# Kernel optimization log

Measured on AMD Instinct MI355X. Metric: run time of the kernel, lower is better.

## Reference

```python
import jax, jax.numpy as jnp
import numpy as np

NUM_INPUTS = 100          # nodes 0..99 have no in-edges (consume x)
NUM_HIDDEN = 501          # nodes 100..600, each with fan-in 4
FAN_IN = 4


def _make_edges():
    # Deterministic DAG: hidden node i = 100+k draws 4 distinct predecessors from [0, i)
    rs = np.random.RandomState(42)
    rows = np.stack([rs.choice(NUM_INPUTS + k, size=FAN_IN, replace=False)
                     for k in range(NUM_HIDDEN)]).astype(np.int32)
    return jnp.asarray(rows)


def setup_inputs() -> dict:
    key = jax.random.key(0)
    k_x, k_wi, k_bi, k_wh, k_bh = jax.random.split(key, 5)
    s = 1.0 / np.sqrt(FAN_IN)
    return {
        "x": jax.random.normal(k_x, (NUM_INPUTS,), dtype=jnp.float32),
        "w_in": jax.random.uniform(k_wi, (NUM_INPUTS,), jnp.float32, -1.0, 1.0),
        "b_in": jax.random.uniform(k_bi, (NUM_INPUTS,), jnp.float32, -1.0, 1.0),
        "w_hid": jax.random.uniform(k_wh, (NUM_HIDDEN, FAN_IN), jnp.float32, -s, s),
        "b_hid": jax.random.uniform(k_bh, (NUM_HIDDEN,), jnp.float32, -s, s),
        "edge_idx": _make_edges(),  # [501, 4] int32, row k indexes nodes < 100+k
    }


def reference(x, w_in, b_in, w_hid, b_hid, edge_idx):
    n_in = x.shape[0]
    total = n_in + edge_idx.shape[0]  # 601 nodes
    # Input nodes: sigmoid(Linear(1,1)(x[a])) for each a, vectorized.
    vals_in = jax.nn.sigmoid(w_in * x + b_in)  # [100]
    values = jnp.zeros((total,), x.dtype).at[:n_in].set(vals_in)
    node_ids = jnp.arange(n_in, total)

    def step(values, inp):
        idx, w, b, i = inp
        # cat of predecessor outputs -> Linear(4,1) -> sigmoid
        v = jax.nn.sigmoid(jnp.dot(w, values[idx]) + b)
        return values.at[i].set(v), None

    values, _ = jax.lax.scan(step, values, (edge_idx, w_hid, b_hid, node_ids))
    return values[-1:]  # values[number_of_nodes], shape [1]
```

## Files before the change

kernel.cpp:

```cpp
#include <hip/hip_runtime.h>


#define NUM_IN  100
#define NUM_HID 501
#define TOTAL   601

__launch_bounds__(64, 1)
__global__ void dag_kernel(const float* __restrict__ x,
                           const float* __restrict__ w_in,
                           const float* __restrict__ b_in,
                           const float* __restrict__ w_hid,
                           const float* __restrict__ b_hid,
                           const int*   __restrict__ edge_idx,
                           float* __restrict__ out) {
    __shared__ float vals[TOTAL];
    const int lane = threadIdx.x;

#define LOADP(J)                                                              \
    int4   e##J = make_int4(0, 0, 0, 0);                                      \
    float4 w##J = make_float4(0.f, 0.f, 0.f, 0.f);                            \
    float  b##J = 0.f;                                                        \
    bool   d##J;                                                              \
    {                                                                         \
        int k = (J) * 64 + lane;                                              \
        d##J = (k >= NUM_HID);        \
        if (k < NUM_HID) {                                                    \
            e##J = ((const int4*)edge_idx)[k];                                \
            w##J = ((const float4*)w_hid)[k];                                 \
            b##J = b_hid[k];                                                  \
        }                                                                     \
    }

    LOADP(0) LOADP(1) LOADP(2) LOADP(3) LOADP(4) LOADP(5) LOADP(6) LOADP(7)

    {
        float s = fmaf(w_in[lane], x[lane], b_in[lane]);
        vals[lane] = __builtin_amdgcn_rcpf(1.0f + __expf(-s));
    }
    if (lane < NUM_IN - 64) {
        int i = 64 + lane;
        float s = fmaf(w_in[i], x[i], b_in[i]);
        vals[i] = __builtin_amdgcn_rcpf(1.0f + __expf(-s));
    }
    #pragma unroll
    for (int j = 0; j < 8; ++j) {
        int kk = j * 64 + lane;
        if (kk < NUM_HID) vals[NUM_IN + kk] = -1.0f;
    }
    __builtin_amdgcn_wave_barrier();

#define SLOT(J)                                                               \
    if (!__all((int)d##J)) {                                                  \
        if (!d##J) {                                                          \
            float v0 = vals[e##J.x];                                          \
            float v1 = vals[e##J.y];                                          \
            float v2 = vals[e##J.z];                                          \
            float v3 = vals[e##J.w];                                          \
            int ready = ~((__float_as_int(v0) | __float_as_int(v1) |          \
                           __float_as_int(v2) | __float_as_int(v3))) >> 31;   \
            if (ready & 1) {                                                  \
                float s = fmaf(w##J.x, v0,                                    \
                          fmaf(w##J.y, v1,                                    \
                          fmaf(w##J.z, v2,                                    \
                          fmaf(w##J.w, v3, b##J))));                          \
                vals[NUM_IN + (J) * 64 + lane] =                              \
                    __builtin_amdgcn_rcpf(1.0f + __expf(-s));                 \
                d##J = true;                                                  \
            }                                                                 \
        }                                                                     \
    }                                                                         \
    __builtin_amdgcn_wave_barrier();

    bool alldone = false;
    #pragma unroll 1
    for (int sw = 0; sw < 64 && !alldone; ++sw) {
        SLOT(0) SLOT(1) SLOT(2) SLOT(3) SLOT(4) SLOT(5) SLOT(6) SLOT(7)
        alldone = __all((int)(d0 & d1 & d2 & d3 & d4 & d5 & d6 & d7));
    }

    if (lane == 0) out[0] = vals[TOTAL - 1];
}

extern "C" void kernel_launch(void* const* d_in, const int* in_sizes, int n_in,
                              void* d_out, int out_size, void* d_ws, size_t ws_size,
                              hipStream_t stream) {
    (void)in_sizes; (void)n_in; (void)out_size; (void)d_ws; (void)ws_size;
    const float* x     = (const float*)d_in[0];
    const float* w_in  = (const float*)d_in[1];
    const float* b_in  = (const float*)d_in[2];
    const float* w_hid = (const float*)d_in[3];
    const float* b_hid = (const float*)d_in[4];
    const int*   eidx  = (const int*)d_in[5];
    float*       out   = (float*)d_out;

    dag_kernel<<<dim3(1), dim3(64), 0, stream>>>(x, w_in, b_in, w_hid, b_hid,
                                                 eidx, out);
}
```

Before: 71.21 us.

## Stage edge data in LDS via async loads and process DAG chunk-by-chunk

Edge indices, weights and biases are now copied straight into LDS with global_load_lds instead of being held in 8 sets of registers per lane. The sweep over all 8 slots is replaced by a per-chunk loop that spins on each 64-node chunk until every node in it is resolved, then moves on. Since predecessors always have lower indices, chunks can be finished in order. This removes redundant passes over finished or not-yet-ready slots and lowers register pressure, at the cost of strictly serial chunk processing and some extra LDS reads.

```diff
diff --git a/kernel.cpp b/kernel.cpp
--- a/kernel.cpp
+++ b/kernel.cpp
@@ -13,25 +13,26 @@
                            const float* __restrict__ b_hid,
                            const int*   __restrict__ edge_idx,
                            float* __restrict__ out) {
-    __shared__ float vals[TOTAL];
+    __shared__ __align__(16) float  vals[TOTAL];
+    __shared__ __align__(16) int4   eL[512];
+    __shared__ __align__(16) float4 wL[512];
+    __shared__ __align__(16) float  bL[512];
     const int lane = threadIdx.x;
 
-#define LOADP(J)                                                              \
-    int4   e##J = make_int4(0, 0, 0, 0);                                      \
-    float4 w##J = make_float4(0.f, 0.f, 0.f, 0.f);                            \
-    float  b##J = 0.f;                                                        \
-    bool   d##J;                                                              \
-    {                                                                         \
-        int k = (J) * 64 + lane;                                              \
-        d##J = (k >= NUM_HID);        \
-        if (k < NUM_HID) {                                                    \
-            e##J = ((const int4*)edge_idx)[k];                                \
-            w##J = ((const float4*)w_hid)[k];                                 \
-            b##J = b_hid[k];                                                  \
-        }                                                                     \
+    #pragma unroll 1
+    for (int j = 0; j < 8; ++j) {
+        int k  = j * 64 + lane;
+        int ks = k < NUM_HID ? k : NUM_HID - 1;
+        __builtin_amdgcn_global_load_lds(
+            (const __attribute__((address_space(1))) void*)(edge_idx + ks * 4),
+            (__attribute__((address_space(3))) void*)(eL + j * 64), 16, 0, 0);
+        __builtin_amdgcn_global_load_lds(
+            (const __attribute__((address_space(1))) void*)(w_hid + ks * 4),
+            (__attribute__((address_space(3))) void*)(wL + j * 64), 16, 0, 0);
+        __builtin_amdgcn_global_load_lds(
+            (const __attribute__((address_space(1))) void*)(b_hid + ks),
+            (__attribute__((address_space(3))) void*)(bL + j * 64), 4, 0, 0);
     }
-
-    LOADP(0) LOADP(1) LOADP(2) LOADP(3) LOADP(4) LOADP(5) LOADP(6) LOADP(7)
 
     {
         float s = fmaf(w_in[lane], x[lane], b_in[lane]);
@@ -42,40 +43,44 @@
         float s = fmaf(w_in[i], x[i], b_in[i]);
         vals[i] = __builtin_amdgcn_rcpf(1.0f + __expf(-s));
     }
-    #pragma unroll
+    {
+        float4* vp = (float4*)(vals + NUM_IN);
+        const float4 m1 = make_float4(-1.f, -1.f, -1.f, -1.f);
+        vp[lane] = m1;
+        if (lane < 61) vp[64 + lane] = m1;
+        if (lane == 0) vals[TOTAL - 1] = -1.0f;
+    }
+
+    __syncthreads();
+
+    #pragma unroll 1
     for (int j = 0; j < 8; ++j) {
-        int kk = j * 64 + lane;
-        if (kk < NUM_HID) vals[NUM_IN + kk] = -1.0f;
-    }
-    __builtin_amdgcn_wave_barrier();
-
-#define SLOT(J)                                                               \
-    if (!__all((int)d##J)) {                                                  \
-        if (!d##J) {                                                          \
-            float v0 = vals[e##J.x];                                          \
-            float v1 = vals[e##J.y];                                          \
-            float v2 = vals[e##J.z];                                          \
-            float v3 = vals[e##J.w];                                          \
-            int ready = ~((__float_as_int(v0) | __float_as_int(v1) |          \
-                           __float_as_int(v2) | __float_as_int(v3))) >> 31;   \
-            if (ready & 1) {                                                  \
-                float s = fmaf(w##J.x, v0,                                    \
-                          fmaf(w##J.y, v1,                                    \
-                          fmaf(w##J.z, v2,                                    \
-                          fmaf(w##J.w, v3, b##J))));                          \
-                vals[NUM_IN + (J) * 64 + lane] =                              \
-                    __builtin_amdgcn_rcpf(1.0f + __expf(-s));                 \
-                d##J = true;                                                  \
-            }                                                                 \
-        }                                                                     \
-    }                                                                         \
-    __builtin_amdgcn_wave_barrier();
-
-    bool alldone = false;
-    #pragma unroll 1
-    for (int sw = 0; sw < 64 && !alldone; ++sw) {
-        SLOT(0) SLOT(1) SLOT(2) SLOT(3) SLOT(4) SLOT(5) SLOT(6) SLOT(7)
-        alldone = __all((int)(d0 & d1 & d2 & d3 & d4 & d5 & d6 & d7));
+        int  k    = j * 64 + lane;
+        bool done = (k >= NUM_HID);
+        int4   e = make_int4(0, 0, 0, 0);
+        float4 w = make_float4(0.f, 0.f, 0.f, 0.f);
+        float  b = 0.f;
+        if (!done) { e = eL[k]; w = wL[k]; b = bL[k]; }
+        while (!__all((int)done)) {
+            if (!done) {
+                float v0 = vals[e.x];
+                float v1 = vals[e.y];
+                float v2 = vals[e.z];
+                float v3 = vals[e.w];
+                int ns = __float_as_int(v0) | __float_as_int(v1) |
+                         __float_as_int(v2) | __float_as_int(v3);
+                if (ns >= 0) {
+                    float s = fmaf(w.x, v0,
+                              fmaf(w.y, v1,
+                              fmaf(w.z, v2,
+                              fmaf(w.w, v3, b))));
+                    vals[NUM_IN + k] =
+                        __builtin_amdgcn_rcpf(1.0f + __expf(-s));
+                    done = true;
+                }
+            }
+            __builtin_amdgcn_wave_barrier();
+        }
     }
 
     if (lane == 0) out[0] = vals[TOTAL - 1];
```

After: 66.28 us. -6.9%, faster.
